# Kernel tuning notes

Hardware: AMD Instinct MI355X
Metric: run time of the kernel (lower is better)

The kernel has to match this reference:

```python
import jax, jax.numpy as jnp
import numpy as np

POOL = 4
SCALE = 1.0 / 16.0
B, C, H, W = 64, 256, 36, 36
NC = POOL * POOL           # 16 correlation channels
RED = 4                    # SE reduction
INTER = NC // 2            # non-local inter channels = 8


def _hat_cumint(t):
    # integral of hat kernel max(0,1-|s|) over (-inf, t]
    t = jnp.clip(t, -1.0, 1.0)
    return jnp.where(t < 0.0, 0.5 * (t + 1.0) ** 2, 1.0 - 0.5 * (1.0 - t) ** 2)


def _axis_weights(lo, hi, n):
    # lo, hi: (B, P) bin edges in feature coords -> (B, P, n) exact integral
    # of the bilinear (hat) basis of each integer sample i over [lo, hi].
    i = jnp.arange(n, dtype=lo.dtype)
    return _hat_cumint(hi[..., None] - i) - _hat_cumint(lo[..., None] - i)


def prroi_pool(feat, rois_xyxy, pool, scale):
    # Precise RoI Pooling: analytic integral of bilinear interpolation per bin.
    Bn, Cn, Hn, Wn = feat.shape
    x1 = rois_xyxy[:, 0] * scale
    y1 = rois_xyxy[:, 1] * scale
    x2 = rois_xyxy[:, 2] * scale
    y2 = rois_xyxy[:, 3] * scale
    bw = (x2 - x1) / pool
    bh = (y2 - y1) / pool
    k = jnp.arange(pool, dtype=feat.dtype)
    ax = x1[:, None] + k * bw[:, None]
    bx = ax + bw[:, None]
    ay = y1[:, None] + k * bh[:, None]
    by = ay + bh[:, None]
    Wx = _axis_weights(ax, bx, Wn)   # (B, P, W)
    Wy = _axis_weights(ay, by, Hn)   # (B, P, H)
    pooled = jnp.einsum('bchw,bph,bqw->bcpq', feat, Wy, Wx)
    area = (bw * bh)[:, None, None, None]
    return jnp.where(area > 0, pooled / jnp.maximum(area, 1e-12), 0.0)


def setup_inputs() -> dict:
    key = jax.random.key(0)
    ks = jax.random.split(key, 12)
    feat1 = jax.random.normal(ks[0], (B, C, H, W), jnp.float32)
    feat2 = jax.random.normal(ks[1], (B, C, H, W), jnp.float32)
    # valid (x, y, w, h) boxes inside a 576px image
    xy = jax.random.uniform(ks[2], (B, 2), jnp.float32, 0.0, 416.0)
    wh = jax.random.uniform(ks[3], (B, 2), jnp.float32, 32.0, 160.0)
    bb1 = jnp.concatenate([xy, wh], axis=1)[None]  # (1, B, 4)

    def conv_init(k, shape):  # normal(0, sqrt(2/(kh*kw*out)))
        n = shape[0]  # 1x1 convs: kh*kw*out_ch = out_ch
        return jax.random.normal(k, shape, jnp.float32) * np.sqrt(2.0 / n)

    se_w1 = conv_init(ks[4], (NC // RED, NC))
    se_w2 = conv_init(ks[5], (NC, NC // RED))
    nl_theta_w = conv_init(ks[6], (INTER, NC))
    nl_phi_w = conv_init(ks[7], (INTER, NC))
    nl_g_w = conv_init(ks[8], (INTER, NC))
    nl_W_w = conv_init(ks[9], (NC, INTER))
    zi = jnp.zeros((INTER,), jnp.float32)
    zc = jnp.zeros((NC,), jnp.float32)
    return {
        'feat1': feat1, 'feat2': feat2, 'bb1': bb1,
        'se_w1': se_w1, 'se_w2': se_w2,
        'nl_theta_w': nl_theta_w, 'nl_theta_b': zi,
        'nl_phi_w': nl_phi_w, 'nl_phi_b': zi,
        'nl_g_w': nl_g_w, 'nl_g_b': zi,
        'nl_W_w': nl_W_w, 'nl_W_b': zc,
    }


def reference(feat1, feat2, bb1, se_w1, se_w2, nl_theta_w, nl_theta_b,
              nl_phi_w, nl_phi_b, nl_g_w, nl_g_b, nl_W_w, nl_W_b):
    boxes = bb1[0]  # (B, 4) xywh
    xyxy = jnp.concatenate([boxes[:, :2], boxes[:, :2] + boxes[:, 2:4]], axis=1)
    ker = prroi_pool(feat1, xyxy, POOL, SCALE)          # (B, C, P, P)
    Bn, Cn, Hn, Wn = feat2.shape
    kflat = ker.reshape(Bn, Cn, NC)
    # pixel_corr: per-sample 1x1 conv == batched GEMM
    corr = jnp.einsum('bchw,bck->bkhw', feat2, kflat)   # (B, 16, H, W)
    # SE channel attention
    s = corr.mean(axis=(2, 3))                          # (B, 16)
    s = jax.nn.sigmoid(jax.nn.relu(s @ se_w1.T) @ se_w2.T)
    x = corr * s[:, :, None, None]
    # Non-local (embedded gaussian) spatial attention
    xf = x.reshape(Bn, NC, Hn * Wn)                     # (B, 16, N)
    theta = jnp.einsum('oc,bcn->bno', nl_theta_w, xf) + nl_theta_b     # (B, N, 8)
    phi = jnp.einsum('oc,bcn->bon', nl_phi_w, xf) + nl_phi_b[:, None]  # (B, 8, N)
    g = jnp.einsum('oc,bcn->bno', nl_g_w, xf) + nl_g_b                 # (B, N, 8)
    attn = jax.nn.softmax(jnp.einsum('bno,bom->bnm', theta, phi), axis=-1)
    y = jnp.einsum('bnm,bmo->bno', attn, g)             # (B, N, 8)
    z = jnp.einsum('co,bno->bcn', nl_W_w, y) + nl_W_b[:, None]
    return z.reshape(Bn, NC, Hn, Wn) + x
```

## Files before the change

### kernel.cpp

```cpp
#include <hip/hip_runtime.h>
#include <cmath>

#define NB 64
#define NCC 256
#define NH 36
#define NW 36
#define NHW 1296
#define NK 16
#define NI 8
#define SC (1.0f/16.0f)
#define LOG2E 1.4426950408889634f
#define NPAD 1312

typedef __attribute__((ext_vector_type(16))) float f32x16;
typedef __attribute__((ext_vector_type(4)))  float f32x4;
typedef __attribute__((ext_vector_type(4)))  short s16x4;
typedef __attribute__((ext_vector_type(8)))  unsigned short u16x8;
typedef __attribute__((ext_vector_type(2)))  unsigned int u32x2;

__device__ __forceinline__ float hatc(float t){
  t = fminf(fmaxf(t, -1.0f), 1.0f);
  float a = 1.0f + t, bq = 1.0f - t;
  return (t < 0.0f) ? 0.5f*a*a : 1.0f - 0.5f*bq*bq;
}

__device__ __forceinline__ unsigned short bf16rn(float f){
  unsigned int u = __builtin_bit_cast(unsigned int, f);
  return (unsigned short)((u + 0x7FFFu + ((u >> 16) & 1u)) >> 16);
}
__device__ __forceinline__ float bf16tof(unsigned short h){
  unsigned int u = ((unsigned int)h) << 16;
  return __builtin_bit_cast(float, u);
}

__global__ __launch_bounds__(256) void k_prpool(const float* __restrict__ feat1,
    const float* __restrict__ bb1, float* __restrict__ kflat){
  int blk = blockIdx.x;
  int b = blk >> 6, cg = blk & 63;
  int t = threadIdx.x, w = t >> 6, lane = t & 63;
  int c = cg*4 + w;
  __shared__ float4 wY4[36];
  __shared__ float  wXp[36*5];
  float bx = bb1[b*4+0], by = bb1[b*4+1], bwv = bb1[b*4+2], bhv = bb1[b*4+3];
  float x1 = bx*SC, y1 = by*SC;
  float binw = bwv*SC*0.25f, binh = bhv*SC*0.25f;
  if (t < 36){
    float fi = (float)t;
    float4 r;
    r.x = hatc(y1 + 1.0f*binh - fi) - hatc(y1 + 0.0f*binh - fi);
    r.y = hatc(y1 + 2.0f*binh - fi) - hatc(y1 + 1.0f*binh - fi);
    r.z = hatc(y1 + 3.0f*binh - fi) - hatc(y1 + 2.0f*binh - fi);
    r.w = hatc(y1 + 4.0f*binh - fi) - hatc(y1 + 3.0f*binh - fi);
    wY4[t] = r;
  } else if (t < 72){
    int i = t - 36;
    float fi = (float)i;
    wXp[i*5+0] = hatc(x1 + 1.0f*binw - fi) - hatc(x1 + 0.0f*binw - fi);
    wXp[i*5+1] = hatc(x1 + 2.0f*binw - fi) - hatc(x1 + 1.0f*binw - fi);
    wXp[i*5+2] = hatc(x1 + 3.0f*binw - fi) - hatc(x1 + 2.0f*binw - fi);
    wXp[i*5+3] = hatc(x1 + 4.0f*binw - fi) - hatc(x1 + 3.0f*binw - fi);
  }
  __syncthreads();
  f32x4 acc4[4];
  #pragma unroll
  for (int p=0;p<4;p++) acc4[p] = (f32x4){0,0,0,0};
  const float4* fp4 = (const float4*)(feat1 + ((size_t)(b*256+c))*NHW);

  auto body = [&](float4 v, int px){
    #pragma unroll
    for (int j=0;j<4;j++){
      int p = px + j;
      int h = p/36, x = p - h*36;
      float vj = (j==0)?v.x:(j==1)?v.y:(j==2)?v.z:v.w;
      float4 wy = wY4[h];
      f32x4 wxv = {wXp[x*5+0], wXp[x*5+1], wXp[x*5+2], wXp[x*5+3]};
      f32x4 a0 = {vj*wy.x, vj*wy.x, vj*wy.x, vj*wy.x};
      f32x4 a1 = {vj*wy.y, vj*wy.y, vj*wy.y, vj*wy.y};
      f32x4 a2 = {vj*wy.z, vj*wy.z, vj*wy.z, vj*wy.z};
      f32x4 a3 = {vj*wy.w, vj*wy.w, vj*wy.w, vj*wy.w};
      acc4[0] = __builtin_elementwise_fma(a0, wxv, acc4[0]);
      acc4[1] = __builtin_elementwise_fma(a1, wxv, acc4[1]);
      acc4[2] = __builtin_elementwise_fma(a2, wxv, acc4[2]);
      acc4[3] = __builtin_elementwise_fma(a3, wxv, acc4[3]);
    }
  };

  #pragma unroll
  for (int i=0;i<5;i++){
    int f4i = i*64 + lane;
    float4 v = fp4[f4i];
    body(v, f4i*4);
  }
  if (lane < 4){
    int f4i = 320 + lane;
    float4 v = fp4[f4i];
    body(v, f4i*4);
  }
  float accf[16];
  #pragma unroll
  for (int p=0;p<4;p++){
    accf[p*4+0]=acc4[p].x; accf[p*4+1]=acc4[p].y;
    accf[p*4+2]=acc4[p].z; accf[p*4+3]=acc4[p].w;
  }
  #pragma unroll
  for (int k=0;k<16;k++){
    float a = accf[k];
    #pragma unroll
    for (int off=32; off>0; off>>=1) a += __shfl_down(a, off);
    accf[k] = a;
  }
  if (lane == 0){
    float area = binw*binh;
    float ia = (area > 0.0f) ? 1.0f/fmaxf(area,1e-12f) : 0.0f;
    float4* kp = (float4*)(kflat + ((size_t)(b*256+c))*16);
    kp[0] = make_float4(accf[0]*ia, accf[1]*ia, accf[2]*ia, accf[3]*ia);
    kp[1] = make_float4(accf[4]*ia, accf[5]*ia, accf[6]*ia, accf[7]*ia);
    kp[2] = make_float4(accf[8]*ia, accf[9]*ia, accf[10]*ia, accf[11]*ia);
    kp[3] = make_float4(accf[12]*ia, accf[13]*ia, accf[14]*ia, accf[15]*ia);
  }
}

__global__ __launch_bounds__(512) void k_corr(const float* __restrict__ feat2,
    const float* __restrict__ kflat, float* __restrict__ corr,
    float* __restrict__ partial_se){
  int blk = blockIdx.x;
  int b = blk / 6, ch = blk - b*6;
  int t = threadIdx.x, w = t >> 6, lane = t & 63;
  int px0 = ch*216;
  __shared__ float par[4][16][216];

  int wu = __builtin_amdgcn_readfirstlane(w);
  int c0 = wu*32;
  int l4 = (lane < 54) ? lane : 53;

  f32x4 acc[16];
  #pragma unroll
  for (int k=0;k<16;k++) acc[k] = (f32x4){0,0,0,0};

  const float* f2base = feat2 + (size_t)b*NCC*NHW + px0 + l4*4;
  const float* kfb = kflat + (size_t)b*4096;
  #pragma unroll 4
  for (int c = c0; c < c0+32; ++c){
    f32x4 r = *(const f32x4*)(f2base + (size_t)c*NHW);
    f32x16 kf = *(const f32x16*)(kfb + c*16);
    #pragma unroll
    for (int k=0;k<16;k++){
      f32x4 kv = {kf[k], kf[k], kf[k], kf[k]};
      acc[k] = __builtin_elementwise_fma(r, kv, acc[k]);
    }
  }

  if (w >= 4){
    #pragma unroll
    for (int k=0;k<16;k++)
      *(f32x4*)&par[w-4][k][l4*4] = acc[k];
  }
  __syncthreads();
  if (w < 4){
    #pragma unroll
    for (int k=0;k<16;k++){
      f32x4 tmp = *(const f32x4*)&par[w][k][l4*4];
      *(f32x4*)&par[w][k][l4*4] = tmp + acc[k];
    }
  }
  __syncthreads();
  int k = (w<<1) | (lane>>5);
  int j0 = lane & 31;
  float se_r = 0.0f;
  float* cp = corr + (size_t)b*NK*NHW + (size_t)k*NHW + px0;
  for (int jj=j0; jj<54; jj+=32){
    f32x4 s = *(const f32x4*)&par[0][k][jj*4];
    s += *(const f32x4*)&par[1][k][jj*4];
    s += *(const f32x4*)&par[2][k][jj*4];
    s += *(const f32x4*)&par[3][k][jj*4];
    *(f32x4*)(cp + jj*4) = s;
    se_r += (s.x+s.y) + (s.z+s.w);
  }
  #pragma unroll
  for (int off=16; off>0; off>>=1) se_r += __shfl_down(se_r, off, 32);
  if (j0 == 0)
    partial_se[(size_t)blk*16 + k] = se_r;
}

__global__ __launch_bounds__(256) void k_tpg(const float* __restrict__ corr,
    const float* __restrict__ partial_se,
    const float* __restrict__ w1, const float* __restrict__ w2,
    const float* __restrict__ tw, const float* __restrict__ tb,
    const float* __restrict__ pw, const float* __restrict__ pb,
    const float* __restrict__ gw, const float* __restrict__ gb,
    float* __restrict__ sscale,
    unsigned short* __restrict__ thetaX, unsigned short* __restrict__ phiX,
    unsigned short* __restrict__ gT){
  int blk = blockIdx.x;
  int b = blk/6, ch = blk - b*6;
  int t = threadIdx.x;
  __shared__ float Wt[128], Wp[128], Wg[128], Bz[24], Ss[16], sS[16], sR[4];
  if (t < 128){ Wt[t]=tw[t]; Wp[t]=pw[t]; Wg[t]=gw[t]; }
  if (t < 8){ Bz[t]=tb[t]; Bz[8+t]=pb[t]; Bz[16+t]=gb[t]; }
  if (t >= 128 && t < 144){
    int q = t - 128;
    float a = 0.f;
    #pragma unroll
    for (int c2=0; c2<6; c2++) a += partial_se[(size_t)(b*6+c2)*16 + q];
    sS[q] = a * (1.0f/1296.0f);
  }
  __syncthreads();
  if (t < 4){
    float a=0.f;
    #pragma unroll
    for (int k=0;k<16;k++) a += sS[k]*w1[t*16+k];
    sR[t] = fmaxf(a, 0.f);
  }
  __syncthreads();
  if (t < 16){
    float a=0.f;
    #pragma unroll
    for (int j=0;j<4;j++) a += sR[j]*w2[t*4+j];
    float gsc = 1.0f/(1.0f+__expf(-a));
    Ss[t] = gsc;
    if (ch == 0) sscale[b*16+t] = gsc;
  }
  __syncthreads();
  int n = ch*256 + t;
  if (n >= NHW) return;
  float x[16];
  const float* cp = corr + (size_t)b*NK*NHW + n;
  #pragma unroll
  for (int c=0;c<16;c++) x[c] = cp[(size_t)c*NHW] * Ss[c];
  float th[8], ph[8], gg[8];
  #pragma unroll
  for (int o=0;o<8;o++){
    float a=Bz[o], p2=Bz[8+o], gq=Bz[16+o];
    #pragma unroll
    for (int c=0;c<16;c++){
      a  += Wt[o*16+c]*x[c];
      p2 += Wp[o*16+c]*x[c];
      gq += Wg[o*16+c]*x[c];
    }
    th[o]=a*LOG2E; ph[o]=p2; gg[o]=gq;
  }
  unsigned short tH[8], tL[8], pH[8], pL[8];
  #pragma unroll
  for (int o=0;o<8;o++){
    unsigned short hh = bf16rn(th[o]);
    tH[o] = hh; tL[o] = bf16rn(th[o] - bf16tof(hh));
    unsigned short ph2 = bf16rn(ph[o]);
    pH[o] = ph2; pL[o] = bf16rn(ph[o] - bf16tof(ph2));
  }
  {
    u16x8* tp = (u16x8*)(thetaX + ((size_t)b*NPAD + n)*16);
    tp[0] = (u16x8){tH[0],tH[1],tH[2],tH[3], tL[0],tL[1],tL[2],tL[3]};
    tp[1] = (u16x8){tH[4],tH[5],tH[6],tH[7], tL[4],tL[5],tL[6],tL[7]};
    u16x8* pp = (u16x8*)(phiX + ((size_t)b*NPAD + n)*16);
    pp[0] = (u16x8){pH[0],pH[1],pH[2],pH[3], pL[0],pL[1],pL[2],pL[3]};
    pp[1] = (u16x8){pH[4],pH[5],pH[6],pH[7], pL[4],pL[5],pL[6],pL[7]};
  }
  #pragma unroll
  for (int o=0;o<8;o++)
    gT[((size_t)b*16 + o)*NPAD + n] = bf16rn(gg[o]);
  gT[((size_t)b*16 + 8)*NPAD + n] = 0x3F80;
}

__global__ __launch_bounds__(128) void k_attn_part(
    const unsigned short* __restrict__ thetaX, const unsigned short* __restrict__ phiX,
    const unsigned short* __restrict__ gT,
    float* __restrict__ mpart, float* __restrict__ Ypart){
  int blk = blockIdx.x;
  int b = blk / 82, rem = blk - b*82;
  int qb = rem >> 1, kh = rem & 1;
  int t = threadIdx.x, w = t >> 6, lane = t & 63;
  int h = lane >> 5, r31 = lane & 31;
  __shared__ float smm[2][32];
  __shared__ float sY[5][64];
  __shared__ float yl[32][12];

  const unsigned short* thx = thetaX + (size_t)b*NPAD*16;
  const unsigned short* phx = phiX   + (size_t)b*NPAD*16;

  s16x4 Bh, Bl;
  {
    const s16x4* tp = (const s16x4*)(thx + ((size_t)(qb*32 + r31))*16 + h*8);
    Bh = tp[0]; Bl = tp[1];
  }

  int kbeg = kh ? 21 : 0;
  int kend = kh ? 41 : 21;
  int kmid = kh ? 31 : 11;
  int kt0 = w ? kmid : kbeg;
  int ktN = w ? kend : kmid;

  float m = -1e30f;
  f32x16 Y = (f32x16)(0.0f);
  int colc = (r31 < 9) ? r31 : 0;
  const unsigned short* gb2 = gT + ((size_t)b*16 + colc)*NPAD;

  {
    const unsigned short* prow = phx + (size_t)(kt0*32 + r31)*16 + h*8;
    const unsigned short* vrow = gb2 + kt0*32;
    for (int kt = kt0; kt < ktN; ++kt){
      const s16x4* pr = (const s16x4*)prow;
      s16x4 Ah = pr[0], Al = pr[1];
      f32x16 S = __builtin_amdgcn_mfma_f32_32x32x8bf16_1k(Ah, Bl, (f32x16)(0.0f), 0, 0, 0);
      S = __builtin_amdgcn_mfma_f32_32x32x8bf16_1k(Al, Bh, S, 0, 0, 0);
      S = __builtin_amdgcn_mfma_f32_32x32x8bf16_1k(Ah, Bh, S, 0, 0, 0);
      if (kt == 40){
        #pragma unroll
        for (int r=8;r<16;r++) S[r] = -1e30f;
      }
      float a0 = fmaxf(S[0],S[1]),  a1 = fmaxf(S[2],S[3]);
      float a2 = fmaxf(S[4],S[5]),  a3 = fmaxf(S[6],S[7]);
      float a4 = fmaxf(S[8],S[9]),  a5 = fmaxf(S[10],S[11]);
      float a6 = fmaxf(S[12],S[13]),a7 = fmaxf(S[14],S[15]);
      float b0 = fmaxf(a0,a1), b1 = fmaxf(a2,a3);
      float b2 = fmaxf(a4,a5), b3 = fmaxf(a6,a7);
      float tm = fmaxf(fmaxf(b0,b1), fmaxf(b2,b3));
      tm = fmaxf(tm, __shfl_xor(tm, 32));
      float mn = fmaxf(m, tm);
      float cf = __builtin_amdgcn_exp2f(m - mn);
      m = mn;
      float p[16];
      #pragma unroll
      for (int r=0;r<16;r++) p[r] = __builtin_amdgcn_exp2f(S[r] - m);
      #pragma unroll
      for (int r=0;r<5;r++) Y[r] *= cf;
      unsigned int c[8];
      #pragma unroll
      for (int i=0;i<8;i++){
        unsigned int cc;
        asm("v_cvt_pk_bf16_f32 %0, %1, %2" : "=v"(cc) : "v"(p[2*i]), "v"(p[2*i+1]));
        c[i] = cc;
      }
      const s16x4* vr = (const s16x4*)(vrow + h*4);
      #pragma unroll
      for (int mf=0; mf<4; ++mf){
        s16x4 Ap = __builtin_bit_cast(s16x4, (u32x2){c[2*mf], c[2*mf+1]});
        s16x4 Vb = vr[mf*2];
        Y = __builtin_amdgcn_mfma_f32_32x32x8bf16_1k(Vb, Ap, Y, 0, 0, 0);
      }
      prow += 512;
      vrow += 32;
    }
  }

  if (h == 0) smm[w][r31] = m;
  __syncthreads();
  float M = fmaxf(smm[0][r31], smm[1][r31]);
  float cfw = __builtin_amdgcn_exp2f(m - M);
  #pragma unroll
  for (int r=0;r<5;r++) Y[r] *= cfw;
  if (w == 0 && h == 0)
    mpart[((size_t)((b*41 + qb)*2 + kh))*32 + r31] = M;
  if (w == 1){
    #pragma unroll
    for (int r=0;r<5;r++) sY[r][lane] = Y[r];
  }
  __syncthreads();
  if (w == 0){
    #pragma unroll
    for (int r=0;r<5;r++) Y[r] += sY[r][lane];
    if (h == 0){
      yl[r31][0]=Y[0]; yl[r31][1]=Y[1]; yl[r31][2]=Y[2]; yl[r31][3]=Y[3];
      yl[r31][8]=Y[4];
    } else {
      yl[r31][4]=Y[0]; yl[r31][5]=Y[1]; yl[r31][6]=Y[2]; yl[r31][7]=Y[3];
    }
  }
  __syncthreads();

  float* yp = Ypart + (size_t)((b*41 + qb)*2 + kh)*288;
  for (int i = t; i < 288; i += 128){
    int q = i / 9, c2 = i - q*9;
    yp[i] = yl[q][c2];
  }
}

__global__ __launch_bounds__(128) void k_attn_fin(
    const float* __restrict__ mpart, const float* __restrict__ Ypart,
    const float* __restrict__ corr, const float* __restrict__ sscale,
    const float* __restrict__ Ww, const float* __restrict__ Wb,
    float* __restrict__ out){
  int blk = blockIdx.x;
  int b = blk / 41, qb = blk - b*41;
  int t = threadIdx.x;
  __shared__ float yl[32][9];
  __shared__ float cf0[32], cf1[32];
  size_t p2 = (size_t)(b*41 + qb)*2;
  if (t < 32){
    float m0 = mpart[p2*32 + t];
    float m1 = mpart[(p2+1)*32 + t];
    float M = fmaxf(m0, m1);
    cf0[t] = __builtin_amdgcn_exp2f(m0 - M);
    cf1[t] = __builtin_amdgcn_exp2f(m1 - M);
  }
  __syncthreads();
  const float* y0 = Ypart + p2*288;
  const float* y1 = Ypart + (p2+1)*288;
  for (int i = t; i < 288; i += 128){
    int q = i / 9;
    ((float*)yl)[i] = y0[i]*cf0[q] + y1[i]*cf1[q];
  }
  __syncthreads();

  int q = t & 31, cg = t >> 5;
  int n = qb*32 + q;
  if (n < NHW){
    float il = 1.0f / yl[q][8];
    float yv[8];
    #pragma unroll
    for (int o=0;o<8;o++) yv[o] = yl[q][o] * il;
    const float* cp = corr + (size_t)b*NK*NHW + n;
    const float* ss = sscale + b*16;
    float* op = out + (size_t)b*NK*NHW + n;
    #pragma unroll
    for (int i=0;i<4;i++){
      int c2 = cg*4 + i;
      float z = Wb[c2];
      #pragma unroll
      for (int o=0;o<8;o++) z += Ww[c2*8+o]*yv[o];
      op[(size_t)c2*NHW] = z + cp[(size_t)c2*NHW]*ss[c2];
    }
  }
}

extern "C" void kernel_launch(void* const* d_in, const int* in_sizes, int n_in,
                              void* d_out, int out_size, void* d_ws, size_t ws_size,
                              hipStream_t stream){
  const float* feat1 = (const float*)d_in[0];
  const float* feat2 = (const float*)d_in[1];
  const float* bb1   = (const float*)d_in[2];
  const float* se_w1 = (const float*)d_in[3];
  const float* se_w2 = (const float*)d_in[4];
  const float* tw    = (const float*)d_in[5];
  const float* tb    = (const float*)d_in[6];
  const float* pw    = (const float*)d_in[7];
  const float* pb    = (const float*)d_in[8];
  const float* gw    = (const float*)d_in[9];
  const float* gb    = (const float*)d_in[10];
  const float* Ww    = (const float*)d_in[11];
  const float* Wb    = (const float*)d_in[12];
  float* out = (float*)d_out;

  float* ws = (float*)d_ws;
  float* kflat      = ws;
  float* corr       = kflat + 64*256*16;
  float* partial_se = corr + (size_t)64*16*1296;
  float* sscale     = partial_se + 64*6*16;
  unsigned short* thetaX = (unsigned short*)(sscale + 64*16);
  unsigned short* phiX   = thetaX + (size_t)64*NPAD*16;
  unsigned short* gT     = phiX   + (size_t)64*NPAD*16;
  float* mpart = (float*)(gT + (size_t)64*16*NPAD);
  float* Ypart = mpart + (size_t)64*41*2*32;

  hipLaunchKernelGGL(k_prpool, dim3(64*64), dim3(256), 0, stream, feat1, bb1, kflat);
  hipLaunchKernelGGL(k_corr, dim3(64*6), dim3(512), 0, stream, feat2, kflat, corr, partial_se);
  hipLaunchKernelGGL(k_tpg, dim3(64*6), dim3(256), 0, stream, corr, partial_se,
                     se_w1, se_w2, tw, tb, pw, pb, gw, gb, sscale, thetaX, phiX, gT);
  hipLaunchKernelGGL(k_attn_part, dim3(64*82), dim3(128), 0, stream,
                     thetaX, phiX, gT, mpart, Ypart);
  hipLaunchKernelGGL(k_attn_fin, dim3(64*41), dim3(128), 0, stream,
                     mpart, Ypart, corr, sscale, Ww, Wb, out);
}
```

Baseline: 101.3 us.

## Separate PrRoI pooling into column reduction over rows then x-weighting via LDS

Each wavefront now stages its channel's 36x36 feature map in shared memory. Each lane owns one column and reduces it over the rows against the four y-bin weights, then multiplies by its four x weights. This replaces the per-pixel 16-FMA outer product, which needed per-element division and shared-memory weight gathers, with a factorised form that does far fewer FMAs. The cost is extra LDS traffic, a block-wide barrier and 28 idle lanes per wavefront.

```diff
diff --git a/kernel.cpp b/kernel.cpp
--- a/kernel.cpp
+++ b/kernel.cpp
@@ -41,6 +41,7 @@
   int c = cg*4 + w;
   __shared__ float4 wY4[36];
   __shared__ float  wXp[36*5];
+  __shared__ float  sfeat[4][1296];
   float bx = bb1[b*4+0], by = bb1[b*4+1], bwv = bb1[b*4+2], bhv = bb1[b*4+3];
   float x1 = bx*SC, y1 = by*SC;
   float binw = bwv*SC*0.25f, binh = bhv*SC*0.25f;
@@ -60,47 +61,37 @@
     wXp[i*5+2] = hatc(x1 + 3.0f*binw - fi) - hatc(x1 + 2.0f*binw - fi);
     wXp[i*5+3] = hatc(x1 + 4.0f*binw - fi) - hatc(x1 + 3.0f*binw - fi);
   }
-  __syncthreads();
-  f32x4 acc4[4];
-  #pragma unroll
-  for (int p=0;p<4;p++) acc4[p] = (f32x4){0,0,0,0};
-  const float4* fp4 = (const float4*)(feat1 + ((size_t)(b*256+c))*NHW);
-
-  auto body = [&](float4 v, int px){
-    #pragma unroll
-    for (int j=0;j<4;j++){
-      int p = px + j;
-      int h = p/36, x = p - h*36;
-      float vj = (j==0)?v.x:(j==1)?v.y:(j==2)?v.z:v.w;
-      float4 wy = wY4[h];
-      f32x4 wxv = {wXp[x*5+0], wXp[x*5+1], wXp[x*5+2], wXp[x*5+3]};
-      f32x4 a0 = {vj*wy.x, vj*wy.x, vj*wy.x, vj*wy.x};
-      f32x4 a1 = {vj*wy.y, vj*wy.y, vj*wy.y, vj*wy.y};
-      f32x4 a2 = {vj*wy.z, vj*wy.z, vj*wy.z, vj*wy.z};
-      f32x4 a3 = {vj*wy.w, vj*wy.w, vj*wy.w, vj*wy.w};
-      acc4[0] = __builtin_elementwise_fma(a0, wxv, acc4[0]);
-      acc4[1] = __builtin_elementwise_fma(a1, wxv, acc4[1]);
-      acc4[2] = __builtin_elementwise_fma(a2, wxv, acc4[2]);
-      acc4[3] = __builtin_elementwise_fma(a3, wxv, acc4[3]);
-    }
-  };
-
-  #pragma unroll
-  for (int i=0;i<5;i++){
-    int f4i = i*64 + lane;
-    float4 v = fp4[f4i];
-    body(v, f4i*4);
-  }
-  if (lane < 4){
-    int f4i = 320 + lane;
-    float4 v = fp4[f4i];
-    body(v, f4i*4);
-  }
+  {
+    const float4* fp4 = (const float4*)(feat1 + ((size_t)(b*256+c))*NHW);
+    float4* sf4 = (float4*)sfeat[w];
+    #pragma unroll
+    for (int i=0;i<5;i++) sf4[i*64+lane] = fp4[i*64+lane];
+    if (lane < 4) sf4[320+lane] = fp4[320+lane];
+  }
+  __syncthreads();
+
+  int x = (lane < 36) ? lane : 0;
+  f32x4 cacc = (f32x4){0,0,0,0};
+  const float* sc = sfeat[w];
+  #pragma unroll 6
+  for (int h2=0; h2<36; ++h2){
+    float v = sc[h2*36 + x];
+    float4 wy = wY4[h2];
+    f32x4 wyv = {wy.x, wy.y, wy.z, wy.w};
+    f32x4 vv = {v, v, v, v};
+    cacc = __builtin_elementwise_fma(vv, wyv, cacc);
+  }
+  if (lane >= 36) cacc = (f32x4){0,0,0,0};
+
+  float wx0 = wXp[x*5+0], wx1 = wXp[x*5+1], wx2 = wXp[x*5+2], wx3 = wXp[x*5+3];
   float accf[16];
   #pragma unroll
-  for (int p=0;p<4;p++){
-    accf[p*4+0]=acc4[p].x; accf[p*4+1]=acc4[p].y;
-    accf[p*4+2]=acc4[p].z; accf[p*4+3]=acc4[p].w;
+  for (int ky=0;ky<4;ky++){
+    float cy = cacc[ky];
+    accf[ky*4+0] = cy*wx0;
+    accf[ky*4+1] = cy*wx1;
+    accf[ky*4+2] = cy*wx2;
+    accf[ky*4+3] = cy*wx3;
   }
   #pragma unroll
   for (int k=0;k<16;k++){
```

New measurement: 103.2 us. No clear change (+1.9%).
